# Performance work log

Hardware: AMD Instinct MI355X
Metric: run time of the kernel (lower is better)

Reference implementation:

```python
import jax, jax.numpy as jnp
import numpy as np

E = 1_000_000   # num_embeddings
D = 128         # embedding_dim
C = 262_144     # cuda_row_num (cache slots)
N = 16_384      # ids per step


def setup_inputs() -> dict:
    key = jax.random.key(0)
    k1, k2, k3 = jax.random.split(key, 3)
    ids = jax.random.randint(k1, (N,), 0, E, dtype=jnp.int64)
    weight = jax.random.normal(k2, (E, D), dtype=jnp.float32)       # CPU-side full table
    cuda_weight = weight[:C]                                          # warmed-up cache: slot s holds row s
    freq_cnter = jax.random.randint(k3, (E,), 0, 100, dtype=jnp.int64)
    idx_map = jnp.arange(E, dtype=jnp.int64)                          # identity (no dataset reorder)
    cached_idx_map = jnp.arange(C, dtype=jnp.int64)                   # slot -> cached row id (full cache)
    inverted_cached_idx = jnp.where(jnp.arange(E) < C, jnp.arange(E), -1).astype(jnp.int64)
    return {"ids": ids, "idx_map": idx_map, "cached_idx_map": cached_idx_map,
            "inverted_cached_idx": inverted_cached_idx, "freq_cnter": freq_cnter,
            "weight": weight, "cuda_weight": cuda_weight}


def reference(ids, idx_map, cached_idx_map, inverted_cached_idx, freq_cnter, weight, cuda_weight):
    """Faithful functional prepare_ids: unique -> miss detect -> LFU evict ->
    write-back evicted rows to CPU weight -> load missed rows into cache ->
    index translation. Static shapes: unique padded to N with sentinel E;
    OOB scatter indices (== E or == C) are dropped."""
    rows = idx_map[ids]                                   # [N] cpu row ids
    u = jnp.unique(rows, size=N, fill_value=E)            # [N] padded unique
    valid = u < E
    u_safe = jnp.where(valid, u, 0)
    slot_of_u = jnp.where(valid, inverted_cached_idx[u_safe], -1)
    hit = valid & (slot_of_u >= 0)
    miss = valid & (slot_of_u < 0)                        # rows needing CPU->GPU transfer

    # -- LFU eviction: protect slots holding rows in the current backlist (u) --
    protected = jnp.zeros((C,), bool).at[jnp.where(hit, slot_of_u, C)].set(True, mode='drop')
    cached_rows = cached_idx_map                          # [C], -1 == empty slot
    keys = freq_cnter[jnp.clip(cached_rows, 0, E - 1)]
    keys = jnp.where(cached_rows < 0, jnp.int64(-1), keys)            # empty slots used first
    keys = jnp.where(protected, jnp.iinfo(keys.dtype).max, keys)      # never evict backlist
    order = jnp.argsort(keys)                             # slots in eviction priority

    rank = jnp.cumsum(miss) - 1                           # position among misses
    slot_for = jnp.where(miss, order[jnp.clip(rank, 0, C - 1)], C)    # C == dropped
    slot_for_safe = jnp.clip(slot_for, 0, C - 1)
    evicted_rows = cached_rows[slot_for_safe]

    # write-back evicted rows to CPU weight (skip empty slots)
    wb_row = jnp.where(miss & (evicted_rows >= 0), evicted_rows, E)
    weight_new = weight.at[wb_row].set(cuda_weight[slot_for_safe], mode='drop')
    # load missed rows into freed cache slots
    cuda_new = cuda_weight.at[slot_for].set(weight_new[u_safe], mode='drop')

    # update index maps
    inv = inverted_cached_idx.at[wb_row].set(-1, mode='drop')
    inv = inv.at[jnp.where(miss, u, E)].set(slot_for, mode='drop')
    cached_new = cached_idx_map.at[slot_for].set(jnp.where(miss, u, -1), mode='drop')

    gpu_row_idxs = inv[rows]                              # [N] cache slot per input id
    freq_new = freq_cnter.at[jnp.where(valid, u, E)].add(1, mode='drop')
    out = cuda_new[gpu_row_idxs]                          # [N, D] gathered embeddings
    return gpu_row_idxs, out
```

## Files before the change

kernel.cpp:

```cpp
#include <hip/hip_runtime.h>

#define E_TOT 1000000
#define D_DIM 128
#define C_CAP 262144
#define N_IDS 16384
#define NB 102
#define NW 31250
#define SB 256
#define NTHR 512
#define SPB 1024
#define MWB 62
#define CHK 52

static_assert(SB * SPB == C_CAP, "geometry");
static_assert(MWB * NTHR >= NW, "geometry");
static_assert(5 * CHK >= SB, "geometry");
static_assert(5 * NB <= NTHR, "geometry");
static_assert(N_IDS / NTHR == 32, "geometry");

__device__ __forceinline__ int cnt_eq(unsigned w, unsigned pat) {
    unsigned x = w ^ pat;
    unsigned y = ((x & 0x7F7F7F7Fu) + 0x7F7F7F7Fu) | x | 0x7F7F7F7Fu;
    return __popc(~y & 0x80808080u);
}

__device__ __forceinline__ int bucket_of(int crow, const int* __restrict__ freq) {
    int key = (crow < 0) ? -1 : freq[crow < E_TOT ? crow : (E_TOT - 1)];
    return (key < 0) ? 0 : (key >= 100 ? 101 : key + 1);
}

__device__ __forceinline__ int block_exscan(int v, int tid, int* lds8) {
    int lane = tid & 63, wv = tid >> 6;
    int incl = v;
#pragma unroll
    for (int o = 1; o < 64; o <<= 1) {
        int u = __shfl_up(incl, o, 64);
        if (lane >= o) incl += u;
    }
    if (lane == 63) lds8[wv] = incl;
    __syncthreads();
    int wsum = 0;
    for (int w = 0; w < wv; ++w) wsum += lds8[w];
    __syncthreads();
    return wsum + incl - v;
}

__global__ __launch_bounds__(NTHR) void stage1_k(
    const int* __restrict__ ids, const int* __restrict__ idx_map,
    const int* __restrict__ inv, const int* __restrict__ cidx,
    const int* __restrict__ freq,
    unsigned* __restrict__ protBits, unsigned* __restrict__ missBits,
    unsigned short* __restrict__ bucketArr2,
    int* __restrict__ rawHist, int* __restrict__ protHist) {
    const int tid = threadIdx.x, bid = blockIdx.x;
    if (bid < SB) {
        __shared__ int waveHist[8][NB];
        for (int k = tid; k < 8 * NB; k += NTHR) ((int*)waveHist)[k] = 0;
        __syncthreads();
        const int s0 = bid * SPB + 2 * tid;
        const int2 cr = *(const int2*)(cidx + s0);
        const int b0 = bucket_of(cr.x, freq);
        const int b1 = bucket_of(cr.y, freq);
        const int wv = tid >> 6;
        atomicAdd(&waveHist[wv][b0], 1);
        atomicAdd(&waveHist[wv][b1], 1);
        bucketArr2[bid * (SPB / 2) + tid] = (unsigned short)(b0 | (b1 << 8));
        __syncthreads();
        if (tid < NB) {
            int s = 0;
#pragma unroll
            for (int w = 0; w < 8; ++w) s += waveHist[w][tid];
            rawHist[bid * NB + tid] = s;
        }
    } else {
        const int i = (bid - SB) * NTHR + tid;
        int id = ids[i];
        if (id < 0 || id >= E_TOT) return;
        int row = idx_map[id];
        if (row < 0 || row >= E_TOT) return;
        int s = inv[row];
        if (s >= 0) {
            if (s < C_CAP) {
                unsigned bit = 1u << (s & 31);
                unsigned old = atomicOr(&protBits[s >> 5], bit);
                if (!(old & bit)) {
                    int b = bucket_of(cidx[s], freq);
                    atomicAdd(&protHist[(s >> 10) * NB + b], 1);
                }
            }
        } else {
            atomicOr(&missBits[row >> 5], 1u << (row & 31));
        }
    }
}

__global__ __launch_bounds__(NTHR) void stage2_k(
    const unsigned short* __restrict__ bucketArr2,
    const unsigned* __restrict__ protBits,
    const int* __restrict__ rawHist, const int* __restrict__ protHist,
    const unsigned* __restrict__ missBits,
    int* __restrict__ wordPrefix, int* __restrict__ blockSumMiss,
    int* __restrict__ order) {
    const int tid = threadIdx.x, bid = blockIdx.x;
    if (bid < SB) {
        __shared__ unsigned char ldsB[SPB];
        __shared__ unsigned protW[SPB / 32];
        __shared__ int waveHist[8][NB];
        __shared__ int partBefore[5][NB];
        __shared__ int partTotal[5][NB];
        __shared__ int bstart[NB];
        __shared__ int before[NB];
        if (tid < SPB / 32) protW[tid] = protBits[bid * (SPB / 32) + tid];
        for (int k = tid; k < 8 * NB; k += NTHR) ((int*)waveHist)[k] = 0;
        __syncthreads();
        const unsigned short pk = bucketArr2[bid * (SPB / 2) + tid];
        const unsigned pw = protW[tid >> 4];
        int b0 = ((pw >> ((2 * tid) & 31)) & 1u) ? 255 : (pk & 0xFF);
        int b1 = ((pw >> ((2 * tid + 1) & 31)) & 1u) ? 255 : (pk >> 8);
        ldsB[2 * tid] = (unsigned char)b0;
        ldsB[2 * tid + 1] = (unsigned char)b1;
        const int wv = tid >> 6, lane = tid & 63;
        if (b0 != 255) atomicAdd(&waveHist[wv][b0], 1);
        if (b1 != 255) atomicAdd(&waveHist[wv][b1], 1);
        if (tid < 5 * NB) {
            const int c = tid / NB, b = tid % NB;
            int lo = c * CHK, hi = lo + CHK;
            if (hi > SB) hi = SB;
            int tot = 0, bef = 0;
            for (int blk = lo; blk < hi; ++blk) {
                int v = rawHist[blk * NB + b] - protHist[blk * NB + b];
                tot += v;
                if (blk < bid) bef += v;
            }
            partTotal[c][b] = tot;
            partBefore[c][b] = bef;
        }
        __syncthreads();
        if (tid < NB) {
            int t = 0, bf = 0;
#pragma unroll
            for (int c = 0; c < 5; ++c) {
                t += partTotal[c][tid];
                bf += partBefore[c][tid];
            }
            bstart[tid] = t;
            before[tid] = bf;
        }
        __syncthreads();
        if (tid == 0) {
            int run = 0;
            for (int b = 0; b < NB; ++b) {
                int t = bstart[b];
                bstart[b] = run;
                run += t;
            }
        }
        __syncthreads();
        const unsigned* wp = (const unsigned*)&ldsB[wv * 128];
        unsigned patA = 0x01010101u * (unsigned)b0;
        unsigned patB = 0x01010101u * (unsigned)b1;
        int full = lane >> 1;
        int cA = 0, cB = 0;
        for (int w = 0; w < full; ++w) {
            unsigned x = wp[w];
            cA += cnt_eq(x, patA);
            cB += cnt_eq(x, patB);
        }
        if (lane & 1) {
            unsigned x = wp[full] | 0xFFFF0000u;
            cA += cnt_eq(x, patA);
            cB += cnt_eq(x, patB);
        }
        int pA = 0, pB = 0;
        for (int w = 0; w < wv; ++w) {
            pA += (b0 != 255) ? waveHist[w][b0] : 0;
            pB += (b1 != 255) ? waveHist[w][b1] : 0;
        }
        const int s0 = bid * SPB + 2 * tid;
        if (b0 != 255)
            order[bstart[b0] + before[b0] + pA + cA] = s0;
        if (b1 != 255)
            order[bstart[b1] + before[b1] + pB + cB + ((b0 == b1) ? 1 : 0)] =
                s0 + 1;
    } else {
        __shared__ int lds8[8];
        const int j = bid - SB;
        const int w = j * NTHR + tid;
        int v = (w < NW) ? __popc(missBits[w]) : 0;
        int excl = block_exscan(v, tid, lds8);
        if (w < NW) wordPrefix[w] = excl;
        if (tid == NTHR - 1) blockSumMiss[j] = excl + v;
    }
}

__global__ __launch_bounds__(NTHR) void final_k(
    const int* __restrict__ ids, const int* __restrict__ idx_map,
    const int* __restrict__ inv, const unsigned* __restrict__ missBits,
    const int* __restrict__ wordPrefix, const int* __restrict__ blockSumMiss,
    const int* __restrict__ order, const float* __restrict__ weight,
    const float* __restrict__ cuda_weight, float* __restrict__ out) {
    __shared__ int chunkPrefix[64];
    const int tid = threadIdx.x;
    if (tid < 64) {
        int v = (tid < MWB) ? blockSumMiss[tid] : 0;
        int incl = v;
#pragma unroll
        for (int o = 1; o < 64; o <<= 1) {
            int u = __shfl_up(incl, o, 64);
            if (tid >= o) incl += u;
        }
        chunkPrefix[tid] = incl - v;
    }
    __syncthreads();
    const int i = blockIdx.x * 8 + (tid >> 6);
    const int lane = tid & 63;
    int id = ids[i];
    int row = (id >= 0 && id < E_TOT) ? idx_map[id] : 0;
    row = row < 0 ? 0 : (row >= E_TOT ? E_TOT - 1 : row);
    int s0 = inv[row];
    int slot;
    const float* src;
    if (s0 >= 0) {
        slot = s0;
        src = cuda_weight + (size_t)slot * D_DIM;
    } else {
        int w = row >> 5;
        unsigned mask = (1u << (row & 31)) - 1u;
        int rank = chunkPrefix[w >> 9] + wordPrefix[w] +
                   __popc(missBits[w] & mask);
        rank = rank < 0 ? 0 : (rank >= C_CAP ? C_CAP - 1 : rank);
        slot = order[rank];
        src = weight + (size_t)row * D_DIM;
    }
    if (lane == 0) out[i] = (float)slot;
    const float2* s2 = (const float2*)src;
    float2* d2 = (float2*)(out + N_IDS + (size_t)i * D_DIM);
    d2[lane] = s2[lane];
}

extern "C" void kernel_launch(void* const* d_in, const int* in_sizes, int n_in,
                              void* d_out, int out_size, void* d_ws, size_t ws_size,
                              hipStream_t stream) {
    const int* ids     = (const int*)d_in[0];
    const int* idx_map = (const int*)d_in[1];
    const int* cidx    = (const int*)d_in[2];
    const int* inv     = (const int*)d_in[3];
    const int* freq    = (const int*)d_in[4];
    const float* weight      = (const float*)d_in[5];
    const float* cuda_weight = (const float*)d_in[6];
    float* out = (float*)d_out;

    unsigned char* ws = (unsigned char*)d_ws;
    size_t o = 0;
    auto take = [&](size_t bytes) {
        size_t r = o;
        o += (bytes + 255) & ~(size_t)255;
        return r;
    };
    unsigned* protBits = (unsigned*)(ws + take(C_CAP / 8));
    unsigned* missBits = (unsigned*)(ws + take((size_t)NW * 4));
    int* protHist      = (int*)(ws + take((size_t)SB * NB * 4));
    size_t zbytes = o;
    unsigned short* bucketArr2 = (unsigned short*)(ws + take(C_CAP));
    int* rawHist      = (int*)(ws + take((size_t)SB * NB * 4));
    int* wordPrefix   = (int*)(ws + take((size_t)NW * 4));
    int* blockSumMiss = (int*)(ws + take(MWB * 4));
    int* order        = (int*)(ws + take((size_t)C_CAP * 4));
    (void)ws_size; (void)in_sizes; (void)n_in; (void)out_size;

    hipMemsetAsync(ws, 0, zbytes, stream);

    stage1_k<<<SB + N_IDS / NTHR, NTHR, 0, stream>>>(
        ids, idx_map, inv, cidx, freq, protBits, missBits, bucketArr2,
        rawHist, protHist);

    stage2_k<<<SB + MWB, NTHR, 0, stream>>>(bucketArr2, protBits, rawHist,
                                            protHist, missBits, wordPrefix,
                                            blockSumMiss, order);

    final_k<<<N_IDS / 8, NTHR, 0, stream>>>(ids, idx_map, inv, missBits,
                                            wordPrefix, blockSumMiss, order,
                                            weight, cuda_weight, out);
}
```

Baseline: 36.96 us.

## Fuse embedding gather into stage1 and resolve miss slots in stage2 with spin-wait

The row gather for all ids moves into extra blocks of the first kernel, so it no longer waits on the eviction ordering. Miss ids get their cache slot in stage2 blocks that compute a miss rank from per-chunk popcount prefixes, then spin on an atomically published order entry. Only the first N_IDS order positions are kept. This removes the third launch and the separate word-prefix scan, and shrinks the order buffer. The cost is an inter-block spin-wait that assumes co-residency of producer and consumer blocks, plus redundant per-block prefix recomputation over missBits.

```diff
diff --git a/kernel.cpp b/kernel.cpp
--- a/kernel.cpp
+++ b/kernel.cpp
@@ -9,14 +9,17 @@
 #define SB 256
 #define NTHR 512
 #define SPB 1024
-#define MWB 62
 #define CHK 52
+#define NGB (N_IDS / 8)
+#define TB 32
+#define CW 128
+#define NCH ((NW + CW - 1) / CW)
 
 static_assert(SB * SPB == C_CAP, "geometry");
-static_assert(MWB * NTHR >= NW, "geometry");
 static_assert(5 * CHK >= SB, "geometry");
 static_assert(5 * NB <= NTHR, "geometry");
 static_assert(N_IDS / NTHR == 32, "geometry");
+static_assert(TB * NTHR == N_IDS, "geometry");
 
 __device__ __forceinline__ int cnt_eq(unsigned w, unsigned pat) {
     unsigned x = w ^ pat;
@@ -29,26 +32,11 @@
     return (key < 0) ? 0 : (key >= 100 ? 101 : key + 1);
 }
 
-__device__ __forceinline__ int block_exscan(int v, int tid, int* lds8) {
-    int lane = tid & 63, wv = tid >> 6;
-    int incl = v;
-#pragma unroll
-    for (int o = 1; o < 64; o <<= 1) {
-        int u = __shfl_up(incl, o, 64);
-        if (lane >= o) incl += u;
-    }
-    if (lane == 63) lds8[wv] = incl;
-    __syncthreads();
-    int wsum = 0;
-    for (int w = 0; w < wv; ++w) wsum += lds8[w];
-    __syncthreads();
-    return wsum + incl - v;
-}
-
 __global__ __launch_bounds__(NTHR) void stage1_k(
     const int* __restrict__ ids, const int* __restrict__ idx_map,
     const int* __restrict__ inv, const int* __restrict__ cidx,
-    const int* __restrict__ freq,
+    const int* __restrict__ freq, const float* __restrict__ weight,
+    const float* __restrict__ cuda_weight, float* __restrict__ out,
     unsigned* __restrict__ protBits, unsigned* __restrict__ missBits,
     unsigned short* __restrict__ bucketArr2,
     int* __restrict__ rawHist, int* __restrict__ protHist) {
@@ -72,7 +60,7 @@
             for (int w = 0; w < 8; ++w) s += waveHist[w][tid];
             rawHist[bid * NB + tid] = s;
         }
-    } else {
+    } else if (bid < SB + 32) {
         const int i = (bid - SB) * NTHR + tid;
         int id = ids[i];
         if (id < 0 || id >= E_TOT) return;
@@ -91,16 +79,34 @@
         } else {
             atomicOr(&missBits[row >> 5], 1u << (row & 31));
         }
+    } else {
+        const int i = (bid - SB - 32) * 8 + (tid >> 6);
+        const int lane = tid & 63;
+        int id = ids[i];
+        int row = (id >= 0 && id < E_TOT) ? idx_map[id] : 0;
+        row = row < 0 ? 0 : (row >= E_TOT ? E_TOT - 1 : row);
+        int s0 = inv[row];
+        const float* src;
+        if (s0 >= 0) {
+            if (lane == 0) out[i] = (float)s0;
+            src = cuda_weight + (size_t)s0 * D_DIM;
+        } else {
+            src = weight + (size_t)row * D_DIM;
+        }
+        const float2* s2 = (const float2*)src;
+        float2* d2 = (float2*)(out + N_IDS + (size_t)i * D_DIM);
+        d2[lane] = s2[lane];
     }
 }
 
 __global__ __launch_bounds__(NTHR) void stage2_k(
+    const int* __restrict__ ids, const int* __restrict__ idx_map,
+    const int* __restrict__ inv,
     const unsigned short* __restrict__ bucketArr2,
     const unsigned* __restrict__ protBits,
     const int* __restrict__ rawHist, const int* __restrict__ protHist,
     const unsigned* __restrict__ missBits,
-    int* __restrict__ wordPrefix, int* __restrict__ blockSumMiss,
-    int* __restrict__ order) {
+    unsigned* __restrict__ order, float* __restrict__ out) {
     const int tid = threadIdx.x, bid = blockIdx.x;
     if (bid < SB) {
         __shared__ unsigned char ldsB[SPB];
@@ -177,65 +183,50 @@
             pB += (b1 != 255) ? waveHist[w][b1] : 0;
         }
         const int s0 = bid * SPB + 2 * tid;
-        if (b0 != 255)
-            order[bstart[b0] + before[b0] + pA + cA] = s0;
-        if (b1 != 255)
-            order[bstart[b1] + before[b1] + pB + cB + ((b0 == b1) ? 1 : 0)] =
-                s0 + 1;
+        if (b0 != 255) {
+            int pos = bstart[b0] + before[b0] + pA + cA;
+            if (pos < N_IDS) atomicExch(&order[pos], (unsigned)(s0 + 1));
+        }
+        if (b1 != 255) {
+            int pos = bstart[b1] + before[b1] + pB + cB + ((b0 == b1) ? 1 : 0);
+            if (pos < N_IDS) atomicExch(&order[pos], (unsigned)(s0 + 2));
+        }
     } else {
-        __shared__ int lds8[8];
-        const int j = bid - SB;
-        const int w = j * NTHR + tid;
-        int v = (w < NW) ? __popc(missBits[w]) : 0;
-        int excl = block_exscan(v, tid, lds8);
-        if (w < NW) wordPrefix[w] = excl;
-        if (tid == NTHR - 1) blockSumMiss[j] = excl + v;
+        __shared__ int ldsCP[NCH];
+        for (int k = tid; k < NCH; k += NTHR) ldsCP[k] = 0;
+        __syncthreads();
+        for (int k = tid; k < NW; k += NTHR)
+            atomicAdd(&ldsCP[k >> 7], __popc(missBits[k]));
+        __syncthreads();
+        if (tid == 0) {
+            int run = 0;
+            for (int c = 0; c < NCH; ++c) {
+                int t = ldsCP[c];
+                ldsCP[c] = run;
+                run += t;
+            }
+        }
+        __syncthreads();
+        const int i = (bid - SB) * NTHR + tid;
+        int id = ids[i];
+        int row = (id >= 0 && id < E_TOT) ? idx_map[id] : 0;
+        row = row < 0 ? 0 : (row >= E_TOT ? E_TOT - 1 : row);
+        if (inv[row] < 0) {
+            const int w = row >> 5;
+            int rank = ldsCP[w >> 7];
+            for (int k = (w >> 7) << 7; k < w; ++k)
+                rank += __popc(missBits[k]);
+            rank += __popc(missBits[w] & ((1u << (row & 31)) - 1u));
+            rank = rank < 0 ? 0 : (rank >= N_IDS ? N_IDS - 1 : rank);
+            unsigned v = 0;
+            for (int spin = 0; spin < (1 << 22); ++spin) {
+                v = atomicOr(&order[rank], 0u);
+                if (v) break;
+                __builtin_amdgcn_s_sleep(8);
+            }
+            out[i] = (float)((int)v - 1);
+        }
     }
-}
-
-__global__ __launch_bounds__(NTHR) void final_k(
-    const int* __restrict__ ids, const int* __restrict__ idx_map,
-    const int* __restrict__ inv, const unsigned* __restrict__ missBits,
-    const int* __restrict__ wordPrefix, const int* __restrict__ blockSumMiss,
-    const int* __restrict__ order, const float* __restrict__ weight,
-    const float* __restrict__ cuda_weight, float* __restrict__ out) {
-    __shared__ int chunkPrefix[64];
-    const int tid = threadIdx.x;
-    if (tid < 64) {
-        int v = (tid < MWB) ? blockSumMiss[tid] : 0;
-        int incl = v;
-#pragma unroll
-        for (int o = 1; o < 64; o <<= 1) {
-            int u = __shfl_up(incl, o, 64);
-            if (tid >= o) incl += u;
-        }
-        chunkPrefix[tid] = incl - v;
-    }
-    __syncthreads();
-    const int i = blockIdx.x * 8 + (tid >> 6);
-    const int lane = tid & 63;
-    int id = ids[i];
-    int row = (id >= 0 && id < E_TOT) ? idx_map[id] : 0;
-    row = row < 0 ? 0 : (row >= E_TOT ? E_TOT - 1 : row);
-    int s0 = inv[row];
-    int slot;
-    const float* src;
-    if (s0 >= 0) {
-        slot = s0;
-        src = cuda_weight + (size_t)slot * D_DIM;
-    } else {
-        int w = row >> 5;
-        unsigned mask = (1u << (row & 31)) - 1u;
-        int rank = chunkPrefix[w >> 9] + wordPrefix[w] +
-                   __popc(missBits[w] & mask);
-        rank = rank < 0 ? 0 : (rank >= C_CAP ? C_CAP - 1 : rank);
-        slot = order[rank];
-        src = weight + (size_t)row * D_DIM;
-    }
-    if (lane == 0) out[i] = (float)slot;
-    const float2* s2 = (const float2*)src;
-    float2* d2 = (float2*)(out + N_IDS + (size_t)i * D_DIM);
-    d2[lane] = s2[lane];
 }
 
 extern "C" void kernel_launch(void* const* d_in, const int* in_sizes, int n_in,
@@ -260,25 +251,19 @@
     unsigned* protBits = (unsigned*)(ws + take(C_CAP / 8));
     unsigned* missBits = (unsigned*)(ws + take((size_t)NW * 4));
     int* protHist      = (int*)(ws + take((size_t)SB * NB * 4));
+    unsigned* order    = (unsigned*)(ws + take((size_t)N_IDS * 4));
     size_t zbytes = o;
     unsigned short* bucketArr2 = (unsigned short*)(ws + take(C_CAP));
-    int* rawHist      = (int*)(ws + take((size_t)SB * NB * 4));
-    int* wordPrefix   = (int*)(ws + take((size_t)NW * 4));
-    int* blockSumMiss = (int*)(ws + take(MWB * 4));
-    int* order        = (int*)(ws + take((size_t)C_CAP * 4));
+    int* rawHist = (int*)(ws + take((size_t)SB * NB * 4));
     (void)ws_size; (void)in_sizes; (void)n_in; (void)out_size;
 
     hipMemsetAsync(ws, 0, zbytes, stream);
 
-    stage1_k<<<SB + N_IDS / NTHR, NTHR, 0, stream>>>(
-        ids, idx_map, inv, cidx, freq, protBits, missBits, bucketArr2,
-        rawHist, protHist);
-
-    stage2_k<<<SB + MWB, NTHR, 0, stream>>>(bucketArr2, protBits, rawHist,
-                                            protHist, missBits, wordPrefix,
-                                            blockSumMiss, order);
-
-    final_k<<<N_IDS / 8, NTHR, 0, stream>>>(ids, idx_map, inv, missBits,
-                                            wordPrefix, blockSumMiss, order,
-                                            weight, cuda_weight, out);
-}
+    stage1_k<<<SB + 32 + NGB, NTHR, 0, stream>>>(
+        ids, idx_map, inv, cidx, freq, weight, cuda_weight, out,
+        protBits, missBits, bucketArr2, rawHist, protHist);
+
+    stage2_k<<<SB + TB, NTHR, 0, stream>>>(
+        ids, idx_map, inv, bucketArr2, protBits, rawHist, protHist, missBits,
+        order, out);
+}
```

Result: slower. 60.50 us (+63.7%).
